# Kernel optimization log

Hardware: AMD Instinct MI355X
Metric: run time of the kernel (lower is better)

Reference implementation:

```python
import jax, jax.numpy as jnp
import numpy as np

D_MODEL = 1024
D_INNER = 2048      # expand=2 * d_model
HEADDIM = 64
NHEADS = D_INNER // HEADDIM   # 32 (ssm heads)
D_STATE = 128
D_CONV = 4
CHUNK = 256
D_IN_PROJ = 2 * D_INNER + 2 * D_STATE + NHEADS
CONV_DIM = D_INNER + 2 * D_STATE


def setup_inputs() -> dict:
    key = jax.random.key(0)
    ks = jax.random.split(key, 8)
    sc = lambda f: 1.0 / np.sqrt(f)
    dt_init = jax.random.uniform(ks[3], (NHEADS,), minval=0.001, maxval=0.1)
    return {
        "x": jax.random.normal(ks[0], (2, 4096, D_MODEL), jnp.float32),
        "W_in": jax.random.normal(ks[1], (D_MODEL, D_IN_PROJ), jnp.float32) * sc(D_MODEL),
        "conv_w": jax.random.normal(ks[2], (CONV_DIM, D_CONV), jnp.float32) * sc(D_CONV),
        "conv_b": jnp.zeros((CONV_DIM,), jnp.float32),
        "dt_bias": jnp.log(jnp.expm1(dt_init)),            # inverse softplus
        "A_log": jnp.log(jax.random.uniform(ks[4], (NHEADS,), minval=1.0, maxval=16.0)),
        "D": jnp.ones((NHEADS,), jnp.float32),
        "norm_w": jnp.ones((D_INNER,), jnp.float32),
        "W_out": jax.random.normal(ks[5], (D_INNER, D_MODEL), jnp.float32) * sc(D_INNER),
    }


def _segsum(a):
    # a: (..., T) -> (..., T, T) lower-triangular segment sums, -inf above diag
    T = a.shape[-1]
    cs = jnp.cumsum(a, axis=-1)
    diff = cs[..., :, None] - cs[..., None, :]
    mask = jnp.tril(jnp.ones((T, T), bool))
    return jnp.where(mask, diff, -jnp.inf)


def _ssd(x, A, B, C):
    # x: (b,L,h,p) already scaled by dt; A: (b,L,h) = dt*A_head; B,C: (b,L,n)
    b, L, h, p = x.shape
    nc = L // CHUNK
    xc = x.reshape(b, nc, CHUNK, h, p)
    Ac = A.reshape(b, nc, CHUNK, h).transpose(0, 3, 1, 2)      # (b,h,nc,cl)
    Bc = B.reshape(b, nc, CHUNK, -1)
    Cc = C.reshape(b, nc, CHUNK, -1)
    Acs = jnp.cumsum(Ac, axis=-1)
    # intra-chunk (diagonal) term
    Ldec = jnp.exp(_segsum(Ac))                                # (b,h,nc,cl,cl)
    Yd = jnp.einsum('bcln,bcsn,bhcls,bcshp->bclhp', Cc, Bc, Ldec, xc)
    # chunk end states
    decay_states = jnp.exp(Acs[..., -1:] - Acs)                # (b,h,nc,cl)
    states = jnp.einsum('bcln,bhcl,bclhp->bchpn', Bc, decay_states, xc)
    # inter-chunk recurrence (zero initial state)
    states = jnp.concatenate([jnp.zeros_like(states[:, :1]), states], axis=1)
    A_chunk = jnp.pad(Acs[..., -1], ((0, 0), (0, 0), (1, 0)))  # (b,h,nc+1)
    decay_chunk = jnp.exp(_segsum(A_chunk))                    # (b,h,nc+1,nc+1)
    states = jnp.einsum('bhzc,bchpn->bzhpn', decay_chunk, states)[:, :-1]
    # state -> output term
    out_decay = jnp.exp(Acs)                                   # (b,h,nc,cl)
    Yo = jnp.einsum('bcln,bchpn,bhcl->bclhp', Cc, states, out_decay)
    return (Yd + Yo).reshape(b, L, h, p)


def reference(x, W_in, conv_w, conv_b, dt_bias, A_log, D, norm_w, W_out):
    b, L, _ = x.shape
    zxbcdt = x @ W_in                                          # (b,L,4384)
    z, xBC, dt = jnp.split(zxbcdt, [D_INNER, 2 * D_INNER + 2 * D_STATE], axis=-1)
    # causal depthwise conv1d + silu
    xp = jnp.pad(xBC, ((0, 0), (D_CONV - 1, 0), (0, 0)))
    conv = sum(xp[:, k:k + L] * conv_w[:, k] for k in range(D_CONV)) + conv_b
    xBC = jax.nn.silu(conv)
    xs, B, C = jnp.split(xBC, [D_INNER, D_INNER + D_STATE], axis=-1)
    dt = jax.nn.softplus(dt + dt_bias)                         # (b,L,h)
    A = -jnp.exp(A_log)                                        # (h,)
    xh = xs.reshape(b, L, NHEADS, HEADDIM)
    y = _ssd(xh * dt[..., None], dt * A, B, C)                 # (b,L,h,p)
    y = y + xh * D[None, None, :, None]                        # D skip per head
    y = y.reshape(b, L, D_INNER)
    # gated RMSNorm
    u = y * jax.nn.silu(z)
    u = u * jax.lax.rsqrt(jnp.mean(u * u, axis=-1, keepdims=True) + 1e-5) * norm_w
    return u @ W_out
```

## Files before the change

### kernel.cpp

```cpp
#include <hip/hip_runtime.h>
#include <math.h>

#define B_ 2
#define L_ 4096
#define DM 1024
#define DI 2048
#define HD 64
#define NH 32
#define DS 128
#define CH 256
#define NC 16
#define DPROJ 4384
#define CONVD 2304
#define NGEMM 4352

typedef unsigned short u16;
typedef unsigned int u32;
typedef __attribute__((ext_vector_type(8))) short bf16x8;
typedef __attribute__((ext_vector_type(4))) float f32x4;

__device__ __forceinline__ float silu_(float x) { return x / (1.0f + __expf(-x)); }
__device__ __forceinline__ float us2f(u16 u) {
  union { u32 i; float f; } c; c.i = ((u32)u) << 16; return c.f;
}
__device__ __forceinline__ u16 f2us(float f) {
  union { float f; u32 i; } c; c.f = f;
  u32 i = c.i;
  return (u16)((i + 0x7FFFu + ((i >> 16) & 1u)) >> 16);
}
__device__ __forceinline__ void unpack8(uint4 v, float* o) {
  o[0] = us2f(v.x & 0xffffu); o[1] = us2f(v.x >> 16);
  o[2] = us2f(v.y & 0xffffu); o[3] = us2f(v.y >> 16);
  o[4] = us2f(v.z & 0xffffu); o[5] = us2f(v.z >> 16);
  o[6] = us2f(v.w & 0xffffu); o[7] = us2f(v.w >> 16);
}
__device__ __forceinline__ void gload16(const u16* g, u16* l) {
  __builtin_amdgcn_global_load_lds(
      (const __attribute__((address_space(1))) void*)g,
      (__attribute__((address_space(3))) void*)l, 16, 0, 0);
}

__global__ __launch_bounds__(256) void cvt_bf16_k(const float* __restrict__ in,
                                                  u16* __restrict__ out, int n8) {
  int idx = blockIdx.x * 256 + threadIdx.x;
  if (idx >= n8) return;
  const float4 a = *(const float4*)&in[idx * 8];
  const float4 b = *(const float4*)&in[idx * 8 + 4];
  uint4 v;
  v.x = (u32)f2us(a.x) | ((u32)f2us(a.y) << 16);
  v.y = (u32)f2us(a.z) | ((u32)f2us(a.w) << 16);
  v.z = (u32)f2us(b.x) | ((u32)f2us(b.y) << 16);
  v.w = (u32)f2us(b.z) | ((u32)f2us(b.w) << 16);
  *(uint4*)&out[idx * 8] = v;
}

__global__ __launch_bounds__(256) void cvt_t_k(const float* __restrict__ W,
                                               u16* __restrict__ Wt,
                                               int ldW, int ldT) {
  __shared__ float tile[64][65];
  const int t = threadIdx.x;
  const int n0 = blockIdx.x * 64, k0 = blockIdx.y * 64;
#pragma unroll
  for (int i = 0; i < 16; ++i) {
    int j = i * 256 + t;
    int kk = j >> 6, nn = j & 63;
    tile[kk][nn] = W[(size_t)(k0 + kk) * ldW + n0 + nn];
  }
  __syncthreads();
#pragma unroll
  for (int i = 0; i < 16; ++i) {
    int j = i * 256 + t;
    int nn = j >> 6, kk = j & 63;
    Wt[(size_t)(n0 + nn) * ldT + k0 + kk] = f2us(tile[kk][nn]);
  }
}

template <int KDIM, int NTN, int EPI>
__global__ __launch_bounds__(256) void gemm_bf16_k(const u16* __restrict__ A,
                                                   const u16* __restrict__ Bt,
                                                   u16* __restrict__ zb,
                                                   u16* __restrict__ xraw,
                                                   float* __restrict__ outf,
                                                   int nwg) {
  __shared__ u16 pool[(EPI == 1) ? 17408 : 16384];
  u16* Al = pool;
  u16* Bl = pool + 8192;
  const int t = threadIdx.x;
  const int wv = t >> 6, lane = t & 63;
  const int fr = lane & 15, oct = lane >> 4;
  const int wr = wv >> 1, wc = wv & 1;
  const int q = nwg >> 3;
  const int wg = (blockIdx.x & 7) * q + (blockIdx.x >> 3);
  const int bm = wg / NTN, bn = wg % NTN;
  const int m0 = bm * 128, n0 = bn * 128;

  const int lr = lane >> 3, ls = lane & 7;
  const int gslot = (ls ^ lr) * 8;

  f32x4 acc[4][4];
#pragma unroll
  for (int mm = 0; mm < 4; ++mm)
#pragma unroll
    for (int nn = 0; nn < 4; ++nn) acc[mm][nn] = (f32x4){0.f, 0.f, 0.f, 0.f};

  for (int k0 = 0; k0 < KDIM; k0 += 64) {
    if (k0) __syncthreads();
#pragma unroll
    for (int i = 0; i < 4; ++i) {
      const int rowA = wv * 32 + i * 8;
      gload16(&A[(size_t)(m0 + rowA + lr) * KDIM + k0 + gslot], &Al[rowA * 64]);
      gload16(&Bt[(size_t)(n0 + rowA + lr) * KDIM + k0 + gslot], &Bl[rowA * 64]);
    }
    __syncthreads();
#pragma unroll
    for (int kk = 0; kk < 2; ++kk) {
      bf16x8 af[4], bfr[4];
#pragma unroll
      for (int mm = 0; mm < 4; ++mm)
        af[mm] = *(const bf16x8*)&Al[(wr * 64 + mm * 16 + fr) * 64 +
                                     (((kk * 4 + oct) ^ (fr & 7)) * 8)];
#pragma unroll
      for (int nn = 0; nn < 4; ++nn)
        bfr[nn] = *(const bf16x8*)&Bl[(wc * 64 + nn * 16 + fr) * 64 +
                                      (((kk * 4 + oct) ^ (fr & 7)) * 8)];
#pragma unroll
      for (int mm = 0; mm < 4; ++mm)
#pragma unroll
        for (int nn = 0; nn < 4; ++nn)
          acc[mm][nn] = __builtin_amdgcn_mfma_f32_16x16x32_bf16(af[mm], bfr[nn],
                                                                acc[mm][nn], 0, 0, 0);
    }
  }

  if (EPI == 0) {
    const bool isz = (n0 < DI);
#pragma unroll
    for (int P = 0; P < 2; ++P) {
      __syncthreads();
      u16* Oh = pool;
      if (wr == P) {
#pragma unroll
        for (int mm = 0; mm < 4; ++mm)
#pragma unroll
          for (int i = 0; i < 4; ++i) {
            int rloc = mm * 16 + oct * 4 + i;
#pragma unroll
            for (int nn = 0; nn < 4; ++nn)
              Oh[rloc * 136 + wc * 64 + nn * 16 + fr] = f2us(acc[mm][nn][i]);
          }
      }
      __syncthreads();
#pragma unroll
      for (int p = 0; p < 4; ++p) {
        int e = p * 256 + t;
        int row = e >> 4, cs = (e & 15) * 8;
        uint4 v = *(const uint4*)&Oh[row * 136 + cs];
        size_t grow = m0 + P * 64 + row;
        int col = n0 + cs;
        if (isz) *(uint4*)&zb[grow * DI + col] = v;
        else     *(uint4*)&xraw[grow * CONVD + (col - DI)] = v;
      }
    }
  } else {
#pragma unroll
    for (int P = 0; P < 2; ++P) {
      __syncthreads();
      float* Of = (float*)pool;
      if (wr == P) {
#pragma unroll
        for (int mm = 0; mm < 4; ++mm)
#pragma unroll
          for (int i = 0; i < 4; ++i) {
            int rloc = mm * 16 + oct * 4 + i;
#pragma unroll
            for (int nn = 0; nn < 4; ++nn)
              Of[rloc * 132 + wc * 64 + nn * 16 + fr] = acc[mm][nn][i];
          }
      }
      __syncthreads();
#pragma unroll
      for (int p = 0; p < 8; ++p) {
        int e = p * 256 + t;
        int row = e >> 5, c4 = (e & 31) * 4;
        float4 v = *(const float4*)&Of[row * 132 + c4];
        *(float4*)&outf[(size_t)(m0 + P * 64 + row) * DM + n0 + c4] = v;
      }
    }
  }
}

__global__ __launch_bounds__(256) void dt_gemm_k(const float* __restrict__ x,
                                                 const float* __restrict__ W,
                                                 const float* __restrict__ dtb,
                                                 float* __restrict__ dtp) {
  __shared__ float xs[8 * 1024];
  const int t = threadIdx.x;
  const int row0 = blockIdx.x * 8;
#pragma unroll
  for (int i = 0; i < 8; ++i) {
    int j4 = i * 256 + t;
    *(float4*)&xs[j4 * 4] = *(const float4*)&x[(size_t)row0 * DM + j4 * 4];
  }
  __syncthreads();
  const int r = t >> 5, h = t & 31;
  float a0 = 0.f, a1 = 0.f, a2 = 0.f, a3 = 0.f;
  const float* wcol = W + (DI + CONVD) + h;
  const float* xr = &xs[r * 1024];
  for (int k = 0; k < 1024; k += 4) {
    float4 xv = *(const float4*)&xr[k];
    a0 += xv.x * wcol[(size_t)(k + 0) * DPROJ];
    a1 += xv.y * wcol[(size_t)(k + 1) * DPROJ];
    a2 += xv.z * wcol[(size_t)(k + 2) * DPROJ];
    a3 += xv.w * wcol[(size_t)(k + 3) * DPROJ];
  }
  float v = (a0 + a1) + (a2 + a3) + dtb[h];
  dtp[(size_t)(row0 + r) * NH + h] = (v > 20.0f) ? v : log1pf(__expf(v));
}

__global__ __launch_bounds__(256) void conv_silu_k(const u16* __restrict__ xraw,
                                                   const float* __restrict__ cw,
                                                   const float* __restrict__ cb,
                                                   u16* __restrict__ xbc) {
  int idx = blockIdx.x * 256 + threadIdx.x;
  int ch8 = idx % (CONVD / 8);
  int bl = idx / (CONVD / 8);
  int l = bl & (L_ - 1);
  int ch = ch8 * 8;
  const u16* src = xraw + (size_t)bl * CONVD + ch;
  float a[8], o[8];
#pragma unroll
  for (int qq = 0; qq < 8; ++qq) a[qq] = cb[ch + qq];
  float w0[8], w1[8], w2[8], w3[8];
#pragma unroll
  for (int qq = 0; qq < 8; ++qq) {
    float4 w = *(const float4*)&cw[(ch + qq) * 4];
    w0[qq] = w.x; w1[qq] = w.y; w2[qq] = w.z; w3[qq] = w.w;
  }
  if (l >= 3) {
    uint4 v = *(const uint4*)&src[-3 * CONVD]; unpack8(v, o);
#pragma unroll
    for (int qq = 0; qq < 8; ++qq) a[qq] += o[qq] * w0[qq];
  }
  if (l >= 2) {
    uint4 v = *(const uint4*)&src[-2 * CONVD]; unpack8(v, o);
#pragma unroll
    for (int qq = 0; qq < 8; ++qq) a[qq] += o[qq] * w1[qq];
  }
  if (l >= 1) {
    uint4 v = *(const uint4*)&src[-CONVD]; unpack8(v, o);
#pragma unroll
    for (int qq = 0; qq < 8; ++qq) a[qq] += o[qq] * w2[qq];
  }
  {
    uint4 v = *(const uint4*)&src[0]; unpack8(v, o);
#pragma unroll
    for (int qq = 0; qq < 8; ++qq) a[qq] += o[qq] * w3[qq];
  }
  uint4 ov;
  ov.x = (u32)f2us(silu_(a[0])) | ((u32)f2us(silu_(a[1])) << 16);
  ov.y = (u32)f2us(silu_(a[2])) | ((u32)f2us(silu_(a[3])) << 16);
  ov.z = (u32)f2us(silu_(a[4])) | ((u32)f2us(silu_(a[5])) << 16);
  ov.w = (u32)f2us(silu_(a[6])) | ((u32)f2us(silu_(a[7])) << 16);
  *(uint4*)&xbc[(size_t)bl * CONVD + ch] = ov;
}

__global__ __launch_bounds__(256) void acs_k(const float* __restrict__ dtp,
                                             const float* __restrict__ A_log,
                                             float* __restrict__ Acs) {
  const int t = threadIdx.x;
  const int lane = t & 63, wv = t >> 6;
  const int idx = blockIdx.x * 4 + wv;
  const int h = (idx >> 4) & (NH - 1);
  const int c = idx & (NC - 1);
  const int b = idx >> 9;
  const float Ah = -__expf(A_log[h]);
  const size_t base = ((size_t)b * L_ + c * CH + lane * 4) * NH + h;
  float v0 = dtp[base] * Ah;
  float v1 = dtp[base + NH] * Ah;
  float v2 = dtp[base + 2 * NH] * Ah;
  float v3 = dtp[base + 3 * NH] * Ah;
  float c1 = v0 + v1, c2 = c1 + v2, c3 = c2 + v3;
  float tot = c3;
#pragma unroll
  for (int off = 1; off < 64; off <<= 1) {
    float p = __shfl_up(tot, off, 64);
    if (lane >= off) tot += p;
  }
  float excl = tot - c3;
  float4 ov = make_float4(excl + v0, excl + c1, excl + c2, excl + c3);
  *(float4*)&Acs[(size_t)idx * CH + lane * 4] = ov;
}

#define SLP 72
__global__ __launch_bounds__(256) void states_k(const u16* __restrict__ xbc,
                                                const float* __restrict__ dtp,
                                                const float* __restrict__ Acs,
                                                float* __restrict__ states) {
  __shared__ u16 BtT[128 * SLP];
  __shared__ u16 XtT[64 * SLP];
  const int t = threadIdx.x;
  const int wv = t >> 6, lane = t & 63;
  const int fr = lane & 15, oct = lane >> 4;
  const int h = blockIdx.x & 31, c = (blockIdx.x >> 5) & 15, b = blockIdx.x >> 9;
  const size_t acsb = (((size_t)b * NH + h) * NC + c) * CH;
  const float acs_last = Acs[acsb + (CH - 1)];
  const size_t rowbase = (size_t)b * L_ + c * CH;

  f32x4 acc[2][4];
#pragma unroll
  for (int mt = 0; mt < 2; ++mt)
#pragma unroll
    for (int pt = 0; pt < 4; ++pt) acc[mt][pt] = (f32x4){0.f, 0.f, 0.f, 0.f};

  for (int lt = 0; lt < 4; ++lt) {
    __syncthreads();
#pragma unroll
    for (int i = 0; i < 4; ++i) {
      int ci = i * 256 + t;
      int l = ci >> 4, nk = ci & 15;
      uint4 v = *(const uint4*)&xbc[(rowbase + lt * 64 + l) * CONVD + DI + nk * 8];
      u16 p8[8];
      p8[0] = (u16)(v.x & 0xffffu); p8[1] = (u16)(v.x >> 16);
      p8[2] = (u16)(v.y & 0xffffu); p8[3] = (u16)(v.y >> 16);
      p8[4] = (u16)(v.z & 0xffffu); p8[5] = (u16)(v.z >> 16);
      p8[6] = (u16)(v.w & 0xffffu); p8[7] = (u16)(v.w >> 16);
#pragma unroll
      for (int qq = 0; qq < 8; ++qq) {
        int r = nk * 8 + qq;
        BtT[r * SLP + ((((l >> 3) ^ (r >> 3)) & 7) << 3) + (l & 7)] = p8[qq];
      }
    }
#pragma unroll
    for (int i = 0; i < 2; ++i) {
      int ci = i * 256 + t;
      int l = ci >> 3, pk = ci & 7;
      size_t row = rowbase + lt * 64 + l;
      uint4 v = *(const uint4*)&xbc[row * CONVD + h * HD + pk * 8];
      float d = dtp[row * NH + h] * __expf(acs_last - Acs[acsb + lt * 64 + l]);
      float o[8]; unpack8(v, o);
#pragma unroll
      for (int qq = 0; qq < 8; ++qq) {
        int r = pk * 8 + qq;
        XtT[r * SLP + ((((l >> 3) ^ (r >> 3)) & 7) << 3) + (l & 7)] = f2us(o[qq] * d);
      }
    }
    __syncthreads();
#pragma unroll
    for (int ks = 0; ks < 2; ++ks) {
      bf16x8 afr[2], bfr[4];
#pragma unroll
      for (int mt = 0; mt < 2; ++mt) {
        int r = wv * 32 + mt * 16 + fr;
        afr[mt] = *(const bf16x8*)&BtT[r * SLP + ((((ks * 4 + oct) ^ (r >> 3)) & 7) << 3)];
      }
#pragma unroll
      for (int pt = 0; pt < 4; ++pt) {
        int r = pt * 16 + fr;
        bfr[pt] = *(const bf16x8*)&XtT[r * SLP + ((((ks * 4 + oct) ^ (r >> 3)) & 7) << 3)];
      }
#pragma unroll
      for (int mt = 0; mt < 2; ++mt)
#pragma unroll
        for (int pt = 0; pt < 4; ++pt)
          acc[mt][pt] = __builtin_amdgcn_mfma_f32_16x16x32_bf16(afr[mt], bfr[pt],
                                                                acc[mt][pt], 0, 0, 0);
    }
  }
  size_t sbase = (((size_t)b * NC + c) * NH + h) * (size_t)(HD * DS);
#pragma unroll
  for (int mt = 0; mt < 2; ++mt)
#pragma unroll
    for (int pt = 0; pt < 4; ++pt) {
      int p = pt * 16 + fr;
      int n0 = wv * 32 + mt * 16 + oct * 4;
      *(f32x4*)&states[sbase + (size_t)p * DS + n0] = acc[mt][pt];
    }
}

__global__ __launch_bounds__(256) void scan_k(float* __restrict__ states,
                                              const float* __restrict__ Acs) {
  const int t = threadIdx.x;
  const int seg = blockIdx.x & 31;
  const int bh = blockIdx.x >> 5;
  const int h = bh & 31, b = bh >> 5;
  const int elem = seg * 256 + t;
  const size_t acssb = ((size_t)b * NH + h) * NC * CH;
  float run = 0.0f;
#pragma unroll
  for (int c = 0; c < NC; ++c) {
    float dAl = __expf(Acs[acssb + (size_t)c * CH + (CH - 1)]);
    size_t e = (((size_t)b * NC + c) * NH + h) * (size_t)(HD * DS) + elem;
    float s = states[e];
    states[e] = run;
    run = fmaf(dAl, run, s);
  }
}

#define C_OFF 0
#define B_OFF 8192
#define XT_OFF 16384
#define PL_OFF 20992
#define SST_OFF 8192
#define POOL_SZ 25600

__global__ __launch_bounds__(256) void ssd_out_k(const u16* __restrict__ xbc,
                                                 const float* __restrict__ dtp,
                                                 const float* __restrict__ Acs,
                                                 const float* __restrict__ states,
                                                 const float* __restrict__ Dvec,
                                                 u16* __restrict__ y) {
  __shared__ u16 pool[POOL_SZ];
  __shared__ float AcsL[64];
  __shared__ float AcsS[64];
  const int t = threadIdx.x;
  const int wv = t >> 6, lane = t & 63;
  const int lt = blockIdx.x & 3;
  const int h = (blockIdx.x >> 2) & 31;
  const int c = (blockIdx.x >> 7) & 15;
  const int b = blockIdx.x >> 11;
  const size_t acsb = (((size_t)b * NH + h) * NC + c) * CH;
  const size_t rowbase = (size_t)b * L_ + c * CH;

  const int fr = lane & 15;
  const int oct = lane >> 4;
  const int swz = (fr & 7) << 3;

#pragma unroll
  for (int i = 0; i < 4; ++i) {
    int ci = i * 256 + t; int ll = ci >> 4, ck = ci & 15;
    size_t row = rowbase + lt * 64 + ll;
    uint4 v = *(const uint4*)&xbc[row * CONVD + DI + DS + ck * 8];
    *(uint4*)&pool[C_OFF + ll * 128 + ((ck * 8) ^ ((ll & 7) << 3))] = v;
  }
  if (t < 64) AcsL[t] = Acs[acsb + lt * 64 + t];

  f32x4 acc_y[4];
#pragma unroll
  for (int i = 0; i < 4; ++i) acc_y[i] = (f32x4){0.f, 0.f, 0.f, 0.f};

  for (int st = 0; st <= lt; ++st) {
#pragma unroll
    for (int i = 0; i < 4; ++i) {
      int ci = i * 256 + t; int ll = ci >> 4, ck = ci & 15;
      size_t row = rowbase + st * 64 + ll;
      uint4 v = *(const uint4*)&xbc[row * CONVD + DI + ck * 8];
      *(uint4*)&pool[B_OFF + ll * 128 + ((ck * 8) ^ ((ll & 7) << 3))] = v;
    }
#pragma unroll
    for (int i = 0; i < 2; ++i) {
      int ci = i * 256 + t; int s = ci >> 3, pk = ci & 7;
      size_t row = rowbase + st * 64 + s;
      uint4 v = *(const uint4*)&xbc[row * CONVD + h * HD + pk * 8];
      float d = dtp[row * NH + h];
      float o[8]; unpack8(v, o);
#pragma unroll
      for (int qq = 0; qq < 8; ++qq) pool[XT_OFF + (pk * 8 + qq) * 72 + s] = f2us(o[qq] * d);
    }
    if (t < 64) AcsS[t] = Acs[acsb + st * 64 + t];
    __syncthreads();

#pragma unroll
    for (int ss4 = 0; ss4 < 4; ++ss4) {
      f32x4 sacc = (f32x4){0.f, 0.f, 0.f, 0.f};
#pragma unroll
      for (int kk = 0; kk < 4; ++kk) {
        bf16x8 ca = *(const bf16x8*)&pool[C_OFF + (wv * 16 + fr) * 128 + ((kk * 32 + oct * 8) ^ swz)];
        bf16x8 bb = *(const bf16x8*)&pool[B_OFF + (ss4 * 16 + fr) * 128 + ((kk * 32 + oct * 8) ^ swz)];
        sacc = __builtin_amdgcn_mfma_f32_16x16x32_bf16(ca, bb, sacc, 0, 0, 0);
      }
      float aS = AcsS[ss4 * 16 + fr];
      int s_tile = ss4 * 16 + fr;
#pragma unroll
      for (int i = 0; i < 4; ++i) {
        int r = oct * 4 + i;
        int l_tile = wv * 16 + r;
        float aL = AcsL[l_tile];
        float wgt = ((st < lt) || (s_tile <= l_tile)) ? __expf(aL - aS) : 0.0f;
        pool[PL_OFF + wv * 1152 + r * 72 + s_tile] = f2us(sacc[i] * wgt);
      }
    }
#pragma unroll
    for (int pp4 = 0; pp4 < 4; ++pp4) {
#pragma unroll
      for (int kk2 = 0; kk2 < 2; ++kk2) {
        bf16x8 pa = *(const bf16x8*)&pool[PL_OFF + wv * 1152 + fr * 72 + kk2 * 32 + oct * 8];
        bf16x8 xb = *(const bf16x8*)&pool[XT_OFF + (pp4 * 16 + fr) * 72 + kk2 * 32 + oct * 8];
        acc_y[pp4] = __builtin_amdgcn_mfma_f32_16x16x32_bf16(pa, xb, acc_y[pp4], 0, 0, 0);
      }
    }
    __syncthreads();
  }

  {
    size_t sb = (((size_t)b * NC + c) * NH + h) * (size_t)(HD * DS);
#pragma unroll
    for (int i = 0; i < 8; ++i) {
      int ci = i * 256 + t; int p = ci >> 5, nk = ci & 31;
      float4 v = *(const float4*)&states[sb + (size_t)p * DS + nk * 4];
      u32 lo = (u32)f2us(v.x) | ((u32)f2us(v.y) << 16);
      u32 hi = (u32)f2us(v.z) | ((u32)f2us(v.w) << 16);
      *(uint2*)&pool[SST_OFF + p * 136 + nk * 4] = make_uint2(lo, hi);
    }
  }
  __syncthreads();

  f32x4 yo[4];
#pragma unroll
  for (int i = 0; i < 4; ++i) yo[i] = (f32x4){0.f, 0.f, 0.f, 0.f};
#pragma unroll
  for (int pp4 = 0; pp4 < 4; ++pp4) {
#pragma unroll
    for (int kk = 0; kk < 4; ++kk) {
      bf16x8 ca = *(const bf16x8*)&pool[C_OFF + (wv * 16 + fr) * 128 + ((kk * 32 + oct * 8) ^ swz)];
      bf16x8 sbf = *(const bf16x8*)&pool[SST_OFF + (pp4 * 16 + fr) * 136 + kk * 32 + oct * 8];
      yo[pp4] = __builtin_amdgcn_mfma_f32_16x16x32_bf16(ca, sbf, yo[pp4], 0, 0, 0);
    }
  }

  const float Dh = Dvec[h];
#pragma unroll
  for (int i = 0; i < 4; ++i) {
    int l_tile = wv * 16 + oct * 4 + i;
    float eL = __expf(AcsL[l_tile]);
    size_t row = rowbase + lt * 64 + l_tile;
#pragma unroll
    for (int pp4 = 0; pp4 < 4; ++pp4) {
      int col = h * HD + pp4 * 16 + fr;
      float xs = us2f(xbc[row * CONVD + col]);
      float val = acc_y[pp4][i] + eL * yo[pp4][i] + Dh * xs;
      y[row * DI + col] = f2us(val);
    }
  }
}

__global__ __launch_bounds__(256) void gnorm_k(const u16* __restrict__ zb,
                                               const float* __restrict__ nw,
                                               u16* __restrict__ y) {
  const int row = blockIdx.x, t = threadIdx.x;
  const u16* zr = zb + (size_t)row * DI;
  u16* yr = y + (size_t)row * DI;
  uint4 zv = *(const uint4*)&zr[t * 8];
  uint4 yv = *(const uint4*)&yr[t * 8];
  float uz[8], uy[8];
  unpack8(zv, uz); unpack8(yv, uy);
  float u[8], ssum = 0.0f;
#pragma unroll
  for (int j = 0; j < 8; ++j) { u[j] = uy[j] * silu_(uz[j]); ssum += u[j] * u[j]; }
#pragma unroll
  for (int off = 32; off >= 1; off >>= 1) ssum += __shfl_xor(ssum, off, 64);
  __shared__ float red[4];
  if ((t & 63) == 0) red[t >> 6] = ssum;
  __syncthreads();
  float sc = rsqrtf((red[0] + red[1] + red[2] + red[3]) * (1.0f / DI) + 1e-5f);
  float4 w0 = *(const float4*)&nw[t * 8];
  float4 w1 = *(const float4*)&nw[t * 8 + 4];
  float o0 = u[0] * sc * w0.x, o1 = u[1] * sc * w0.y, o2 = u[2] * sc * w0.z, o3 = u[3] * sc * w0.w;
  float o4 = u[4] * sc * w1.x, o5 = u[5] * sc * w1.y, o6 = u[6] * sc * w1.z, o7 = u[7] * sc * w1.w;
  uint4 ov;
  ov.x = (u32)f2us(o0) | ((u32)f2us(o1) << 16);
  ov.y = (u32)f2us(o2) | ((u32)f2us(o3) << 16);
  ov.z = (u32)f2us(o4) | ((u32)f2us(o5) << 16);
  ov.w = (u32)f2us(o6) | ((u32)f2us(o7) << 16);
  *(uint4*)&yr[t * 8] = ov;
}

extern "C" void kernel_launch(void* const* d_in, const int* in_sizes, int n_in,
                              void* d_out, int out_size, void* d_ws, size_t ws_size,
                              hipStream_t stream) {
  const float* x      = (const float*)d_in[0];
  const float* W_in   = (const float*)d_in[1];
  const float* conv_w = (const float*)d_in[2];
  const float* conv_b = (const float*)d_in[3];
  const float* dt_b   = (const float*)d_in[4];
  const float* A_log  = (const float*)d_in[5];
  const float* Dvec   = (const float*)d_in[6];
  const float* norm_w = (const float*)d_in[7];
  const float* W_out  = (const float*)d_in[8];
  float* out = (float*)d_out;

  u16* zb       = (u16*)d_ws;
  u16* xbc      = zb + (size_t)B_ * L_ * DI;
  float* dtp    = (float*)(xbc + (size_t)B_ * L_ * CONVD);
  float* Acs    = dtp + (size_t)B_ * L_ * NH;
  float* states = Acs + (size_t)B_ * NH * L_;
  u16* uni      = (u16*)(states + (size_t)B_ * NC * NH * HD * DS);
  u16* xraw = uni;
  u16* y    = uni;

  u16* xb16   = (u16*)states;
  u16* wint   = xb16 + (size_t)B_ * L_ * DM;
  u16* woutt  = (u16*)states;

  const int Mrows = B_ * L_;

  cvt_bf16_k<<<(Mrows * DM / 8 + 255) / 256, 256, 0, stream>>>(x, xb16, Mrows * DM / 8);
  cvt_t_k<<<dim3(NGEMM / 64, DM / 64), 256, 0, stream>>>(W_in, wint, DPROJ, DM);

  const int nwg_in = (Mrows / 128) * (NGEMM / 128);
  gemm_bf16_k<DM, NGEMM / 128, 0><<<nwg_in, 256, 0, stream>>>(
      xb16, wint, zb, xraw, nullptr, nwg_in);
  dt_gemm_k<<<Mrows / 8, 256, 0, stream>>>(x, W_in, dt_b, dtp);

  conv_silu_k<<<(Mrows * (CONVD / 8)) / 256, 256, 0, stream>>>(xraw, conv_w, conv_b, xbc);
  acs_k<<<(B_ * NH * NC) / 4, 256, 0, stream>>>(dtp, A_log, Acs);
  states_k<<<B_ * NC * NH, 256, 0, stream>>>(xbc, dtp, Acs, states);
  scan_k<<<B_ * NH * 32, 256, 0, stream>>>(states, Acs);
  ssd_out_k<<<B_ * NC * NH * 4, 256, 0, stream>>>(xbc, dtp, Acs, states, Dvec, y);
  gnorm_k<<<Mrows, 256, 0, stream>>>(zb, norm_w, y);

  cvt_t_k<<<dim3(DM / 64, DI / 64), 256, 0, stream>>>(W_out, woutt, DM, DI);
  const int nwg_out = (Mrows / 128) * (DM / 128);
  gemm_bf16_k<DI, DM / 128, 1><<<nwg_out, 256, 0, stream>>>(
      y, woutt, nullptr, nullptr, out, nwg_out);
}
```

Before: 411.7 us.

## Fuse x bf16 cast into dt GEMM, store states in bf16, restructure ssd_out per chunk

Drops the separate fp32-to-bf16 conversion kernel for x and has the dt projection kernel write the bf16 copy while it loads x. Chunk states are now stored as bf16 instead of fp32, which halves the traffic in states_k, scan_k and ssd_out_k, though the scan accumulates through bf16-rounded stored values. ssd_out_k now runs one 512-thread block per (b,chunk,head) instead of four 256-thread blocks. Each block loads the state and C once, folds the exp(Acs) output decay into C before the MFMA, and iterates over all four source sub-tiles with a causal skip per wave. The bf16 state rounding costs some precision in exchange.

```diff
diff --git a/kernel.cpp b/kernel.cpp
--- a/kernel.cpp
+++ b/kernel.cpp
@@ -34,24 +34,16 @@
   o[4] = us2f(v.z & 0xffffu); o[5] = us2f(v.z >> 16);
   o[6] = us2f(v.w & 0xffffu); o[7] = us2f(v.w >> 16);
 }
+__device__ __forceinline__ bf16x8 scale8(bf16x8 a, float s) {
+  bf16x8 r;
+#pragma unroll
+  for (int j = 0; j < 8; ++j) r[j] = (short)f2us(us2f((u16)a[j]) * s);
+  return r;
+}
 __device__ __forceinline__ void gload16(const u16* g, u16* l) {
   __builtin_amdgcn_global_load_lds(
       (const __attribute__((address_space(1))) void*)g,
       (__attribute__((address_space(3))) void*)l, 16, 0, 0);
-}
-
-__global__ __launch_bounds__(256) void cvt_bf16_k(const float* __restrict__ in,
-                                                  u16* __restrict__ out, int n8) {
-  int idx = blockIdx.x * 256 + threadIdx.x;
-  if (idx >= n8) return;
-  const float4 a = *(const float4*)&in[idx * 8];
-  const float4 b = *(const float4*)&in[idx * 8 + 4];
-  uint4 v;
-  v.x = (u32)f2us(a.x) | ((u32)f2us(a.y) << 16);
-  v.y = (u32)f2us(a.z) | ((u32)f2us(a.w) << 16);
-  v.z = (u32)f2us(b.x) | ((u32)f2us(b.y) << 16);
-  v.w = (u32)f2us(b.z) | ((u32)f2us(b.w) << 16);
-  *(uint4*)&out[idx * 8] = v;
 }
 
 __global__ __launch_bounds__(256) void cvt_t_k(const float* __restrict__ W,
@@ -192,14 +184,19 @@
 __global__ __launch_bounds__(256) void dt_gemm_k(const float* __restrict__ x,
                                                  const float* __restrict__ W,
                                                  const float* __restrict__ dtb,
-                                                 float* __restrict__ dtp) {
+                                                 float* __restrict__ dtp,
+                                                 u16* __restrict__ xb16) {
   __shared__ float xs[8 * 1024];
   const int t = threadIdx.x;
   const int row0 = blockIdx.x * 8;
 #pragma unroll
   for (int i = 0; i < 8; ++i) {
     int j4 = i * 256 + t;
-    *(float4*)&xs[j4 * 4] = *(const float4*)&x[(size_t)row0 * DM + j4 * 4];
+    float4 v = *(const float4*)&x[(size_t)row0 * DM + j4 * 4];
+    *(float4*)&xs[j4 * 4] = v;
+    u32 lo = (u32)f2us(v.x) | ((u32)f2us(v.y) << 16);
+    u32 hi = (u32)f2us(v.z) | ((u32)f2us(v.w) << 16);
+    *(uint2*)&xb16[(size_t)row0 * DM + j4 * 4] = make_uint2(lo, hi);
   }
   __syncthreads();
   const int r = t >> 5, h = t & 31;
@@ -295,7 +292,7 @@
 __global__ __launch_bounds__(256) void states_k(const u16* __restrict__ xbc,
                                                 const float* __restrict__ dtp,
                                                 const float* __restrict__ Acs,
-                                                float* __restrict__ states) {
+                                                u16* __restrict__ st16) {
   __shared__ u16 BtT[128 * SLP];
   __shared__ u16 XtT[64 * SLP];
   const int t = threadIdx.x;
@@ -373,164 +370,169 @@
     for (int pt = 0; pt < 4; ++pt) {
       int p = pt * 16 + fr;
       int n0 = wv * 32 + mt * 16 + oct * 4;
-      *(f32x4*)&states[sbase + (size_t)p * DS + n0] = acc[mt][pt];
-    }
-}
-
-__global__ __launch_bounds__(256) void scan_k(float* __restrict__ states,
+      u32 lo = (u32)f2us(acc[mt][pt][0]) | ((u32)f2us(acc[mt][pt][1]) << 16);
+      u32 hi = (u32)f2us(acc[mt][pt][2]) | ((u32)f2us(acc[mt][pt][3]) << 16);
+      *(uint2*)&st16[sbase + (size_t)p * DS + n0] = make_uint2(lo, hi);
+    }
+}
+
+__global__ __launch_bounds__(256) void scan_k(u16* __restrict__ st16,
                                               const float* __restrict__ Acs) {
   const int t = threadIdx.x;
-  const int seg = blockIdx.x & 31;
-  const int bh = blockIdx.x >> 5;
+  const int seg = blockIdx.x & 15;
+  const int bh = blockIdx.x >> 4;
   const int h = bh & 31, b = bh >> 5;
-  const int elem = seg * 256 + t;
+  const int e2 = seg * 256 + t;
   const size_t acssb = ((size_t)b * NH + h) * NC * CH;
-  float run = 0.0f;
+  float run0 = 0.0f, run1 = 0.0f;
 #pragma unroll
   for (int c = 0; c < NC; ++c) {
     float dAl = __expf(Acs[acssb + (size_t)c * CH + (CH - 1)]);
-    size_t e = (((size_t)b * NC + c) * NH + h) * (size_t)(HD * DS) + elem;
-    float s = states[e];
-    states[e] = run;
-    run = fmaf(dAl, run, s);
-  }
-}
-
-#define C_OFF 0
-#define B_OFF 8192
-#define XT_OFF 16384
-#define PL_OFF 20992
-#define SST_OFF 8192
-#define POOL_SZ 25600
-
-__global__ __launch_bounds__(256) void ssd_out_k(const u16* __restrict__ xbc,
-                                                 const float* __restrict__ dtp,
-                                                 const float* __restrict__ Acs,
-                                                 const float* __restrict__ states,
-                                                 const float* __restrict__ Dvec,
-                                                 u16* __restrict__ y) {
-  __shared__ u16 pool[POOL_SZ];
-  __shared__ float AcsL[64];
-  __shared__ float AcsS[64];
+    size_t e = (((size_t)b * NC + c) * NH + h) * (size_t)(HD * DS) + e2 * 2;
+    u32 v = *(const u32*)&st16[e];
+    float s0 = us2f((u16)(v & 0xffffu)), s1 = us2f((u16)(v >> 16));
+    *(u32*)&st16[e] = (u32)f2us(run0) | ((u32)f2us(run1) << 16);
+    run0 = fmaf(dAl, run0, s0);
+    run1 = fmaf(dAl, run1, s1);
+  }
+}
+
+#define SP 72
+#define XOFF 8192
+#define POFF 12800
+__global__ __launch_bounds__(512, 4) void ssd_out_k(const u16* __restrict__ xbc,
+                                                    const float* __restrict__ dtp,
+                                                    const float* __restrict__ Acs,
+                                                    const u16* __restrict__ st16,
+                                                    const float* __restrict__ Dvec,
+                                                    u16* __restrict__ y) {
+  __shared__ u16 pool[31232];
+  __shared__ float acs_s[256];
   const int t = threadIdx.x;
-  const int wv = t >> 6, lane = t & 63;
-  const int lt = blockIdx.x & 3;
-  const int h = (blockIdx.x >> 2) & 31;
-  const int c = (blockIdx.x >> 7) & 15;
-  const int b = blockIdx.x >> 11;
+  const int w = t >> 6, lane = t & 63;
+  const int fr = lane & 15, oct = lane >> 4;
+  const int h = blockIdx.x & 31, c = (blockIdx.x >> 5) & 15, b = blockIdx.x >> 9;
   const size_t acsb = (((size_t)b * NH + h) * NC + c) * CH;
   const size_t rowbase = (size_t)b * L_ + c * CH;
-
-  const int fr = lane & 15;
-  const int oct = lane >> 4;
-  const int swz = (fr & 7) << 3;
-
-#pragma unroll
-  for (int i = 0; i < 4; ++i) {
-    int ci = i * 256 + t; int ll = ci >> 4, ck = ci & 15;
-    size_t row = rowbase + lt * 64 + ll;
-    uint4 v = *(const uint4*)&xbc[row * CONVD + DI + DS + ck * 8];
-    *(uint4*)&pool[C_OFF + ll * 128 + ((ck * 8) ^ ((ll & 7) << 3))] = v;
-  }
-  if (t < 64) AcsL[t] = Acs[acsb + lt * 64 + t];
-
-  f32x4 acc_y[4];
-#pragma unroll
-  for (int i = 0; i < 4; ++i) acc_y[i] = (f32x4){0.f, 0.f, 0.f, 0.f};
-
-  for (int st = 0; st <= lt; ++st) {
-#pragma unroll
-    for (int i = 0; i < 4; ++i) {
-      int ci = i * 256 + t; int ll = ci >> 4, ck = ci & 15;
-      size_t row = rowbase + st * 64 + ll;
-      uint4 v = *(const uint4*)&xbc[row * CONVD + DI + ck * 8];
-      *(uint4*)&pool[B_OFF + ll * 128 + ((ck * 8) ^ ((ll & 7) << 3))] = v;
-    }
+  if (t < 256) acs_s[t] = Acs[acsb + t];
+  const size_t sb = (((size_t)b * NC + c) * NH + h) * (size_t)(HD * DS);
+#pragma unroll
+  for (int i = 0; i < 2; ++i) {
+    int ci = i * 512 + t; int p = ci >> 4, nk = ci & 15;
+    uint4 v = *(const uint4*)&st16[sb + (size_t)p * DS + nk * 8];
+    *(uint4*)&pool[p * 136 + nk * 8] = v;
+  }
+  __syncthreads();
+  bf16x8 ca[2][4];
+#pragma unroll
+  for (int mt = 0; mt < 2; ++mt)
+#pragma unroll
+    for (int kk = 0; kk < 4; ++kk)
+      ca[mt][kk] = *(const bf16x8*)&xbc[(rowbase + w * 32 + mt * 16 + fr) * CONVD +
+                                        DI + DS + kk * 32 + oct * 8];
+  f32x4 acc_y[2][4];
+#pragma unroll
+  for (int mt = 0; mt < 2; ++mt)
+#pragma unroll
+    for (int pp4 = 0; pp4 < 4; ++pp4) acc_y[mt][pp4] = (f32x4){0.f, 0.f, 0.f, 0.f};
+
+  {
+    float eL0 = __expf(acs_s[w * 32 + fr]);
+    float eL1 = __expf(acs_s[w * 32 + 16 + fr]);
+#pragma unroll
+    for (int kk = 0; kk < 4; ++kk) {
+      bf16x8 c0 = scale8(ca[0][kk], eL0);
+      bf16x8 c1 = scale8(ca[1][kk], eL1);
+#pragma unroll
+      for (int pp4 = 0; pp4 < 4; ++pp4) {
+        bf16x8 sf = *(const bf16x8*)&pool[(pp4 * 16 + fr) * 136 + kk * 32 + oct * 8];
+        acc_y[0][pp4] = __builtin_amdgcn_mfma_f32_16x16x32_bf16(c0, sf, acc_y[0][pp4], 0, 0, 0);
+        acc_y[1][pp4] = __builtin_amdgcn_mfma_f32_16x16x32_bf16(c1, sf, acc_y[1][pp4], 0, 0, 0);
+      }
+    }
+  }
+
+  const int stmax = w >> 1, delta = (w & 1) << 5;
+  for (int st = 0; st < 4; ++st) {
+    __syncthreads();
 #pragma unroll
     for (int i = 0; i < 2; ++i) {
-      int ci = i * 256 + t; int s = ci >> 3, pk = ci & 7;
+      int ci = i * 512 + t; int ll = ci >> 4, ck = ci & 15;
+      uint4 v = *(const uint4*)&xbc[(rowbase + st * 64 + ll) * CONVD + DI + ck * 8];
+      *(uint4*)&pool[ll * 128 + ((ck * 8) ^ ((ll & 7) << 3))] = v;
+    }
+    {
+      int s = t >> 3, pk = t & 7;
       size_t row = rowbase + st * 64 + s;
       uint4 v = *(const uint4*)&xbc[row * CONVD + h * HD + pk * 8];
       float d = dtp[row * NH + h];
       float o[8]; unpack8(v, o);
 #pragma unroll
-      for (int qq = 0; qq < 8; ++qq) pool[XT_OFF + (pk * 8 + qq) * 72 + s] = f2us(o[qq] * d);
-    }
-    if (t < 64) AcsS[t] = Acs[acsb + st * 64 + t];
+      for (int qq = 0; qq < 8; ++qq) {
+        int r = pk * 8 + qq;
+        pool[XOFF + r * SP + ((((s >> 3) ^ (r >> 3)) & 7) << 3) + (s & 7)] = f2us(o[qq] * d);
+      }
+    }
     __syncthreads();
-
+    if (st > stmax) continue;
+    const bool diag = (st == stmax);
 #pragma unroll
     for (int ss4 = 0; ss4 < 4; ++ss4) {
-      f32x4 sacc = (f32x4){0.f, 0.f, 0.f, 0.f};
-#pragma unroll
-      for (int kk = 0; kk < 4; ++kk) {
-        bf16x8 ca = *(const bf16x8*)&pool[C_OFF + (wv * 16 + fr) * 128 + ((kk * 32 + oct * 8) ^ swz)];
-        bf16x8 bb = *(const bf16x8*)&pool[B_OFF + (ss4 * 16 + fr) * 128 + ((kk * 32 + oct * 8) ^ swz)];
-        sacc = __builtin_amdgcn_mfma_f32_16x16x32_bf16(ca, bb, sacc, 0, 0, 0);
-      }
-      float aS = AcsS[ss4 * 16 + fr];
-      int s_tile = ss4 * 16 + fr;
-#pragma unroll
-      for (int i = 0; i < 4; ++i) {
-        int r = oct * 4 + i;
-        int l_tile = wv * 16 + r;
-        float aL = AcsL[l_tile];
-        float wgt = ((st < lt) || (s_tile <= l_tile)) ? __expf(aL - aS) : 0.0f;
-        pool[PL_OFF + wv * 1152 + r * 72 + s_tile] = f2us(sacc[i] * wgt);
-      }
-    }
+      bf16x8 bbf[4];
+#pragma unroll
+      for (int kk = 0; kk < 4; ++kk)
+        bbf[kk] = *(const bf16x8*)&pool[(ss4 * 16 + fr) * 128 +
+                                        ((kk * 32 + oct * 8) ^ ((fr & 7) << 3))];
+      int s_in = ss4 * 16 + fr;
+      float aS = acs_s[st * 64 + s_in];
+#pragma unroll
+      for (int mt = 0; mt < 2; ++mt) {
+        f32x4 sacc = (f32x4){0.f, 0.f, 0.f, 0.f};
+#pragma unroll
+        for (int kk = 0; kk < 4; ++kk)
+          sacc = __builtin_amdgcn_mfma_f32_16x16x32_bf16(ca[mt][kk], bbf[kk], sacc, 0, 0, 0);
+#pragma unroll
+        for (int i = 0; i < 4; ++i) {
+          int r = mt * 16 + oct * 4 + i;
+          float aL = acs_s[w * 32 + r];
+          float wgt = (!diag || (s_in <= r + delta)) ? __expf(aL - aS) : 0.0f;
+          pool[POFF + w * 2304 + r * SP + s_in] = f2us(sacc[i] * wgt);
+        }
+      }
+    }
+    bf16x8 pa[2][2];
+#pragma unroll
+    for (int mt = 0; mt < 2; ++mt)
+#pragma unroll
+      for (int k2 = 0; k2 < 2; ++k2)
+        pa[mt][k2] = *(const bf16x8*)&pool[POFF + w * 2304 + (mt * 16 + fr) * SP +
+                                           k2 * 32 + oct * 8];
 #pragma unroll
     for (int pp4 = 0; pp4 < 4; ++pp4) {
-#pragma unroll
-      for (int kk2 = 0; kk2 < 2; ++kk2) {
-        bf16x8 pa = *(const bf16x8*)&pool[PL_OFF + wv * 1152 + fr * 72 + kk2 * 32 + oct * 8];
-        bf16x8 xb = *(const bf16x8*)&pool[XT_OFF + (pp4 * 16 + fr) * 72 + kk2 * 32 + oct * 8];
-        acc_y[pp4] = __builtin_amdgcn_mfma_f32_16x16x32_bf16(pa, xb, acc_y[pp4], 0, 0, 0);
-      }
-    }
-    __syncthreads();
-  }
-
-  {
-    size_t sb = (((size_t)b * NC + c) * NH + h) * (size_t)(HD * DS);
-#pragma unroll
-    for (int i = 0; i < 8; ++i) {
-      int ci = i * 256 + t; int p = ci >> 5, nk = ci & 31;
-      float4 v = *(const float4*)&states[sb + (size_t)p * DS + nk * 4];
-      u32 lo = (u32)f2us(v.x) | ((u32)f2us(v.y) << 16);
-      u32 hi = (u32)f2us(v.z) | ((u32)f2us(v.w) << 16);
-      *(uint2*)&pool[SST_OFF + p * 136 + nk * 4] = make_uint2(lo, hi);
-    }
-  }
-  __syncthreads();
-
-  f32x4 yo[4];
-#pragma unroll
-  for (int i = 0; i < 4; ++i) yo[i] = (f32x4){0.f, 0.f, 0.f, 0.f};
-#pragma unroll
-  for (int pp4 = 0; pp4 < 4; ++pp4) {
-#pragma unroll
-    for (int kk = 0; kk < 4; ++kk) {
-      bf16x8 ca = *(const bf16x8*)&pool[C_OFF + (wv * 16 + fr) * 128 + ((kk * 32 + oct * 8) ^ swz)];
-      bf16x8 sbf = *(const bf16x8*)&pool[SST_OFF + (pp4 * 16 + fr) * 136 + kk * 32 + oct * 8];
-      yo[pp4] = __builtin_amdgcn_mfma_f32_16x16x32_bf16(ca, sbf, yo[pp4], 0, 0, 0);
+      int rx = pp4 * 16 + fr, xg = rx >> 3;
+      bf16x8 xb0 = *(const bf16x8*)&pool[XOFF + rx * SP + (((oct) ^ xg) & 7) * 8];
+      bf16x8 xb1 = *(const bf16x8*)&pool[XOFF + rx * SP + (((4 + oct) ^ xg) & 7) * 8];
+#pragma unroll
+      for (int mt = 0; mt < 2; ++mt) {
+        acc_y[mt][pp4] = __builtin_amdgcn_mfma_f32_16x16x32_bf16(pa[mt][0], xb0, acc_y[mt][pp4], 0, 0, 0);
+        acc_y[mt][pp4] = __builtin_amdgcn_mfma_f32_16x16x32_bf16(pa[mt][1], xb1, acc_y[mt][pp4], 0, 0, 0);
+      }
     }
   }
 
   const float Dh = Dvec[h];
 #pragma unroll
-  for (int i = 0; i < 4; ++i) {
-    int l_tile = wv * 16 + oct * 4 + i;
-    float eL = __expf(AcsL[l_tile]);
-    size_t row = rowbase + lt * 64 + l_tile;
-#pragma unroll
-    for (int pp4 = 0; pp4 < 4; ++pp4) {
-      int col = h * HD + pp4 * 16 + fr;
-      float xs = us2f(xbc[row * CONVD + col]);
-      float val = acc_y[pp4][i] + eL * yo[pp4][i] + Dh * xs;
-      y[row * DI + col] = f2us(val);
-    }
-  }
+  for (int mt = 0; mt < 2; ++mt)
+#pragma unroll
+    for (int i = 0; i < 4; ++i) {
+      size_t row = rowbase + w * 32 + mt * 16 + oct * 4 + i;
+#pragma unroll
+      for (int pp4 = 0; pp4 < 4; ++pp4) {
+        int col = h * HD + pp4 * 16 + fr;
+        float xs = us2f(xbc[row * CONVD + col]);
+        y[row * DI + col] = f2us(acc_y[mt][pp4][i] + Dh * xs);
+      }
+    }
 }
 
 __global__ __launch_bounds__(256) void gnorm_k(const u16* __restrict__ zb,
@@ -582,30 +584,30 @@
   u16* xbc      = zb + (size_t)B_ * L_ * DI;
   float* dtp    = (float*)(xbc + (size_t)B_ * L_ * CONVD);
   float* Acs    = dtp + (size_t)B_ * L_ * NH;
-  float* states = Acs + (size_t)B_ * NH * L_;
-  u16* uni      = (u16*)(states + (size_t)B_ * NC * NH * HD * DS);
+  u16* stregion = (u16*)(Acs + (size_t)B_ * NH * L_);
+  u16* uni      = stregion + (size_t)B_ * NC * NH * HD * DS * 2;
   u16* xraw = uni;
   u16* y    = uni;
 
-  u16* xb16   = (u16*)states;
-  u16* wint   = xb16 + (size_t)B_ * L_ * DM;
-  u16* woutt  = (u16*)states;
+  u16* xb16     = stregion;
+  u16* wint     = stregion + (size_t)B_ * L_ * DM;
+  u16* states16 = stregion;
+  u16* woutt    = stregion;
 
   const int Mrows = B_ * L_;
 
-  cvt_bf16_k<<<(Mrows * DM / 8 + 255) / 256, 256, 0, stream>>>(x, xb16, Mrows * DM / 8);
+  dt_gemm_k<<<Mrows / 8, 256, 0, stream>>>(x, W_in, dt_b, dtp, xb16);
   cvt_t_k<<<dim3(NGEMM / 64, DM / 64), 256, 0, stream>>>(W_in, wint, DPROJ, DM);
 
   const int nwg_in = (Mrows / 128) * (NGEMM / 128);
   gemm_bf16_k<DM, NGEMM / 128, 0><<<nwg_in, 256, 0, stream>>>(
       xb16, wint, zb, xraw, nullptr, nwg_in);
-  dt_gemm_k<<<Mrows / 8, 256, 0, stream>>>(x, W_in, dt_b, dtp);
 
   conv_silu_k<<<(Mrows * (CONVD / 8)) / 256, 256, 0, stream>>>(xraw, conv_w, conv_b, xbc);
   acs_k<<<(B_ * NH * NC) / 4, 256, 0, stream>>>(dtp, A_log, Acs);
-  states_k<<<B_ * NC * NH, 256, 0, stream>>>(xbc, dtp, Acs, states);
-  scan_k<<<B_ * NH * 32, 256, 0, stream>>>(states, Acs);
-  ssd_out_k<<<B_ * NC * NH * 4, 256, 0, stream>>>(xbc, dtp, Acs, states, Dvec, y);
+  states_k<<<B_ * NC * NH, 256, 0, stream>>>(xbc, dtp, Acs, states16);
+  scan_k<<<B_ * NH * 16, 256, 0, stream>>>(states16, Acs);
+  ssd_out_k<<<B_ * NC * NH, 512, 0, stream>>>(xbc, dtp, Acs, states16, Dvec, y);
   gnorm_k<<<Mrows, 256, 0, stream>>>(zb, norm_w, y);
 
   cvt_t_k<<<dim3(DM / 64, DI / 64), 256, 0, stream>>>(W_out, woutt, DM, DI);
```

New measurement: 361.5 us. 1.14x faster.
